# Performance work log

Measured on AMD Instinct MI355X. Metric: run time of the kernel, lower is better.

## Reference

```python
import jax, jax.numpy as jnp
import numpy as np

B, N, C, O, K, D = 32, 2048, 64, 64, 3, 16

def setup_inputs() -> dict:
    key = jax.random.key(0)
    ks = jax.random.split(key, 6)
    x = jax.random.normal(ks[0], (B, N, C), dtype=jnp.float32)
    node_embeddings = jax.random.normal(ks[1], (N, D), dtype=jnp.float32)
    adj_m = jax.random.uniform(ks[2], (N, N), dtype=jnp.float32)
    weights_pool = jax.random.normal(ks[3], (D, K, C, O), dtype=jnp.float32) * 0.1
    bias_pool = jax.random.normal(ks[4], (D, O), dtype=jnp.float32) * 0.1
    sa_weight = jax.random.normal(ks[5], (N, 2 * N), dtype=jnp.float32) * (1.0 / np.sqrt(2 * N))
    return {"x": x, "node_embeddings": node_embeddings, "adj_m": adj_m,
            "weights_pool": weights_pool, "bias_pool": bias_pool, "sa_weight": sa_weight}

def reference(x, node_embeddings, adj_m, weights_pool, bias_pool, sa_weight):
    n = node_embeddings.shape[0]
    # learned adaptive adjacency [N,N]
    supports = jax.nn.softmax(jax.nn.relu(node_embeddings @ node_embeddings.T), axis=1)
    # SpatialAttention: 1x1 conv over 2N channels == matmul with [N,2N] weight
    z = jnp.concatenate([supports, adj_m], axis=1) @ sa_weight.T  # [N,N]
    s2 = jax.nn.sigmoid(z)
    supports = s2 * adj_m + (1.0 - s2) * supports
    # Chebyshev polynomial basis
    support_set = [jnp.eye(n, dtype=supports.dtype), supports]
    for _ in range(2, K):
        support_set.append(2.0 * supports @ support_set[-1] - support_set[-2])
    supports_k = jnp.stack(support_set, axis=0)  # [K,N,N]
    # per-node generated weights/bias from embeddings
    weights = jnp.einsum('nd,dkio->nkio', node_embeddings, weights_pool)  # [N,K,C,O]
    bias = node_embeddings @ bias_pool  # [N,O]
    # graph conv: aggregate then per-node matmul
    x_g = jnp.einsum('knm,bmc->bnkc', supports_k, x)  # [B,N,K,C]
    x_gconv = jnp.einsum('bnki,nkio->bno', x_g, weights) + bias  # [B,N,O]
    return x_gconv
```

## Files before the change

kernel.cpp:

```cpp
#include <hip/hip_runtime.h>


typedef unsigned short u16;
typedef float f32x4 __attribute__((ext_vector_type(4)));
typedef __bf16 bf16x8 __attribute__((ext_vector_type(8)));
typedef unsigned short u16x8 __attribute__((ext_vector_type(8)));

#define PSTRIDE ((size_t)2048 * 2048)

__device__ __forceinline__ u16 f2bf(float f) {
    unsigned u = __float_as_uint(f);
    u += 0x7FFFu + ((u >> 16) & 1u);
    return (u16)(u >> 16);
}
__device__ __forceinline__ float bf2f(u16 h) {
    return __uint_as_float((unsigned)h << 16);
}
__device__ __forceinline__ void gl_lds16(const void* g, void* l) {
    __builtin_amdgcn_global_load_lds(
        (const __attribute__((address_space(1))) unsigned*)g,
        (__attribute__((address_space(3))) unsigned*)l, 16, 0, 0);
}

__global__ __launch_bounds__(256)
void preamble(const float* __restrict__ E, const float* __restrict__ adj,
              const float* __restrict__ saw, const float* __restrict__ x,
              const float* __restrict__ Wp, const float* __restrict__ bp,
              float* __restrict__ zf, u16* __restrict__ Acat,
              u16* __restrict__ sawb, u16* __restrict__ xtT,
              u16* __restrict__ Wpb, float* __restrict__ bias) {
    __shared__ u16 t[64][65];
    __shared__ float Bp[1024];
    const int bid = blockIdx.x, tid = threadIdx.x;

    if (bid < 256) {
        const int c0 = (bid & 31) * 64, r0 = (bid >> 5) * 256;
        const int r = r0 + tid;
        const float4* Er = (const float4*)(E + (size_t)r * 16);
        float4 e0 = Er[0], e1 = Er[1], e2 = Er[2], e3 = Er[3];
        *(float4*)(Bp + tid * 4) = *(const float4*)(E + (size_t)c0 * 16 + tid * 4);
        __syncthreads();
        float* zr = zf + (size_t)r * 2048 + c0;
#pragma unroll
        for (int cc = 0; cc < 4; ++cc) {
            float acc[16];
#pragma unroll
            for (int c = 0; c < 16; ++c) {
                const float* bp = Bp + (cc * 16 + c) * 16;
                float s = 0.f;
                s = fmaf(e0.x, bp[0], s);  s = fmaf(e0.y, bp[1], s);
                s = fmaf(e0.z, bp[2], s);  s = fmaf(e0.w, bp[3], s);
                s = fmaf(e1.x, bp[4], s);  s = fmaf(e1.y, bp[5], s);
                s = fmaf(e1.z, bp[6], s);  s = fmaf(e1.w, bp[7], s);
                s = fmaf(e2.x, bp[8], s);  s = fmaf(e2.y, bp[9], s);
                s = fmaf(e2.z, bp[10], s); s = fmaf(e2.w, bp[11], s);
                s = fmaf(e3.x, bp[12], s); s = fmaf(e3.y, bp[13], s);
                s = fmaf(e3.z, bp[14], s); s = fmaf(e3.w, bp[15], s);
                acc[c] = fmaxf(s, 0.f);
            }
#pragma unroll
            for (int q = 0; q < 4; ++q)
                *(float4*)(zr + cc * 16 + q * 4) =
                    make_float4(acc[q * 4], acc[q * 4 + 1], acc[q * 4 + 2], acc[q * 4 + 3]);
        }
    } else if (bid < 4352) {
        size_t j = ((size_t)(bid - 256) * 256 + tid) * 4;
        float4 v = *(const float4*)(adj + j);
        int n = (int)(j >> 11), c = (int)(j & 2047);
        ushort4 o = make_ushort4(f2bf(v.x), f2bf(v.y), f2bf(v.z), f2bf(v.w));
        *(ushort4*)(Acat + (size_t)n * 4096 + 2048 + c) = o;
    } else if (bid < 12544) {
        size_t j = ((size_t)(bid - 4352) * 256 + tid) * 4;
        float4 v = *(const float4*)(saw + j);
        ushort4 o = make_ushort4(f2bf(v.x), f2bf(v.y), f2bf(v.z), f2bf(v.w));
        *(ushort4*)(sawb + j) = o;
    } else if (bid < 13568) {
        int local = bid - 12544;
        int m0 = (local & 31) * 64, b = local >> 5;
        int c = tid & 63, g = tid >> 6;
#pragma unroll
        for (int r = 0; r < 16; ++r) {
            int mm = g * 16 + r;
            t[mm][c] = f2bf(x[((size_t)b * 2048 + m0 + mm) * 64 + c]);
        }
        __syncthreads();
#pragma unroll
        for (int r = 0; r < 16; ++r) {
            int cc = g * 16 + r;
            xtT[((size_t)b * 64 + cc) * 2048 + m0 + c] = t[c][cc];
        }
    } else {
        int local = bid - 13568;
        if (local < 16) {
            const int d = local;
            const float* base = Wp + (size_t)d * 12288;
            for (int idx = tid; idx < 12288; idx += 256) {
                int o = idx / 192, ki = idx - o * 192;
                int k = ki >> 6, i = ki & 63;
                float v;
                if (k == 0)      v = base[i * 64 + o] - base[2 * 4096 + i * 64 + o];
                else if (k == 1) v = base[4096 + i * 64 + o];
                else             v = 2.f * base[2 * 4096 + i * 64 + o];
                Wpb[(size_t)(d * 64 + o) * 192 + ki] = f2bf(v);
            }
        } else {
            const int nb = local - 16;
#pragma unroll
            for (int it = 0; it < 8; ++it) {
                int idx = tid + it * 256;
                int n = nb * 32 + (idx >> 6), o = idx & 63;
                float s = 0.f;
#pragma unroll
                for (int d = 0; d < 16; ++d) s = fmaf(E[n * 16 + d], bp[d * 64 + o], s);
                bias[(size_t)n * 64 + o] = s;
            }
        }
    }
}

__global__ __launch_bounds__(256)
void softmax_rows(const float* __restrict__ zf, u16* __restrict__ Acat) {
    __shared__ float red[4];
    const int n = blockIdx.x, tid = threadIdx.x;
    const int lane = tid & 63, wave = tid >> 6;
    const float* zr = zf + (size_t)n * 2048;
    float4 a = *(const float4*)(zr + tid * 8);
    float4 b = *(const float4*)(zr + tid * 8 + 4);
    float mx = fmaxf(fmaxf(fmaxf(a.x, a.y), fmaxf(a.z, a.w)),
                     fmaxf(fmaxf(b.x, b.y), fmaxf(b.z, b.w)));
    for (int off = 32; off; off >>= 1) mx = fmaxf(mx, __shfl_down(mx, off, 64));
    if (lane == 0) red[wave] = mx;
    __syncthreads();
    mx = fmaxf(fmaxf(red[0], red[1]), fmaxf(red[2], red[3]));
    __syncthreads();
    float v[8] = {__expf(a.x - mx), __expf(a.y - mx), __expf(a.z - mx), __expf(a.w - mx),
                  __expf(b.x - mx), __expf(b.y - mx), __expf(b.z - mx), __expf(b.w - mx)};
    float sum = v[0] + v[1] + v[2] + v[3] + v[4] + v[5] + v[6] + v[7];
    for (int off = 32; off; off >>= 1) sum += __shfl_down(sum, off, 64);
    if (lane == 0) red[wave] = sum;
    __syncthreads();
    sum = red[0] + red[1] + red[2] + red[3];
    float inv = 1.f / sum;
    u16* orow = Acat + (size_t)n * 4096 + tid * 8;
    *(ushort4*)orow = make_ushort4(f2bf(v[0] * inv), f2bf(v[1] * inv),
                                   f2bf(v[2] * inv), f2bf(v[3] * inv));
    *(ushort4*)(orow + 4) = make_ushort4(f2bf(v[4] * inv), f2bf(v[5] * inv),
                                         f2bf(v[6] * inv), f2bf(v[7] * inv));
}

__global__ __launch_bounds__(256, 3)
void gemm_bt(const u16* __restrict__ A, const u16* __restrict__ Bt,
             u16* __restrict__ Cp, int M, int N, int K, int Kh) {
    __shared__ alignas(16) u16 As[128 * 64];
    __shared__ alignas(16) u16 Bs[128 * 64];
    const int tid = threadIdx.x, lane = tid & 63, wave = tid >> 6;
    const int m0 = blockIdx.y * 128, n0 = blockIdx.x * 128;
    const int wm = (wave >> 1) * 64, wn = (wave & 1) * 64;
    const int kbeg = blockIdx.z * Kh, kend = kbeg + Kh;
    const int ml = lane & 15, c0l = lane >> 4;
    f32x4 acc[4][4] = {};

    int baseA[4], mskA[4], baseB[4], mskB[4];
#pragma unroll
    for (int i = 0; i < 4; ++i) { int m = wm + i * 16 + ml; baseA[i] = m * 8; mskA[i] = m & 7; }
#pragma unroll
    for (int j = 0; j < 4; ++j) { int nn = wn + j * 16 + ml; baseB[j] = nn * 8; mskB[j] = nn & 7; }

    for (int k0 = kbeg; k0 < kend; k0 += 64) {
#pragma unroll
        for (int r = 0; r < 4; ++r) {
            int s = wave * 64 + r * 256 + lane;
            int row = s >> 3, gc = (s & 7) ^ (row & 7);
            gl_lds16(A + (size_t)(m0 + row) * K + k0 + gc * 8, As + (size_t)s * 8);
        }
#pragma unroll
        for (int r = 0; r < 4; ++r) {
            int s = wave * 64 + r * 256 + lane;
            int row = s >> 3, gc = (s & 7) ^ (row & 7);
            gl_lds16(Bt + (size_t)(n0 + row) * K + k0 + gc * 8, Bs + (size_t)s * 8);
        }
        __syncthreads();
#pragma unroll
        for (int ks4 = 0; ks4 < 8; ks4 += 4) {
            bf16x8 af[4], bv[4];
#pragma unroll
            for (int i = 0; i < 4; ++i)
                af[i] = *(const bf16x8*)(As + (baseA[i] + ((c0l + ks4) ^ mskA[i])) * 8);
#pragma unroll
            for (int j = 0; j < 4; ++j)
                bv[j] = *(const bf16x8*)(Bs + (baseB[j] + ((c0l + ks4) ^ mskB[j])) * 8);
#pragma unroll
            for (int i = 0; i < 4; ++i)
#pragma unroll
                for (int j = 0; j < 4; ++j)
                    acc[i][j] = __builtin_amdgcn_mfma_f32_16x16x32_bf16(af[i], bv[j], acc[i][j], 0, 0, 0);
        }
        __syncthreads();
    }

    const int col_l = lane & 15, row_l = (lane >> 4) * 4;
    u16* Cz = Cp + (size_t)blockIdx.z * M * N;
#pragma unroll
    for (int i = 0; i < 4; ++i)
#pragma unroll
        for (int j = 0; j < 4; ++j)
#pragma unroll
            for (int r = 0; r < 4; ++r) {
                int row = m0 + wm + i * 16 + row_l + r;
                int col = n0 + wn + j * 16 + col_l;
                Cz[(size_t)row * N + col] = f2bf(acc[i][j][r]);
            }
}

__global__ __launch_bounds__(256)
void reduce_z(const u16* __restrict__ p, const u16* __restrict__ Acat,
              u16* __restrict__ S) {
    size_t j = ((size_t)blockIdx.x * 256 + threadIdx.x) * 4;
    ushort4 p0 = *(const ushort4*)(p + j);
    ushort4 p1 = *(const ushort4*)(p + PSTRIDE + j);
    ushort4 p2 = *(const ushort4*)(p + 2 * PSTRIDE + j);
    ushort4 p3 = *(const ushort4*)(p + 3 * PSTRIDE + j);
    int row = (int)(j >> 11), col = (int)(j & 2047);
    ushort4 sp = *(const ushort4*)(Acat + (size_t)row * 4096 + col);
    ushort4 ad = *(const ushort4*)(Acat + (size_t)row * 4096 + 2048 + col);
    float z0 = bf2f(p0.x) + bf2f(p1.x) + bf2f(p2.x) + bf2f(p3.x);
    float z1 = bf2f(p0.y) + bf2f(p1.y) + bf2f(p2.y) + bf2f(p3.y);
    float z2 = bf2f(p0.z) + bf2f(p1.z) + bf2f(p2.z) + bf2f(p3.z);
    float z3 = bf2f(p0.w) + bf2f(p1.w) + bf2f(p2.w) + bf2f(p3.w);
    float s0 = 1.f / (1.f + __expf(-z0)), s1 = 1.f / (1.f + __expf(-z1));
    float s2 = 1.f / (1.f + __expf(-z2)), s3 = 1.f / (1.f + __expf(-z3));
    ushort4 o = make_ushort4(
        f2bf(s0 * bf2f(ad.x) + (1.f - s0) * bf2f(sp.x)),
        f2bf(s1 * bf2f(ad.y) + (1.f - s1) * bf2f(sp.y)),
        f2bf(s2 * bf2f(ad.z) + (1.f - s2) * bf2f(sp.z)),
        f2bf(s3 * bf2f(ad.w) + (1.f - s3) * bf2f(sp.w)));
    *(ushort4*)(S + j) = o;
}

__global__ __launch_bounds__(256)
void reduceT(const u16* __restrict__ p, u16* __restrict__ xg1b,
             u16* __restrict__ xg1T) {
    __shared__ u16 t[64][68];
    int bx = blockIdx.x * 64, by = blockIdx.y * 64;
    int cg = threadIdx.x & 15, rg = threadIdx.x >> 4;
    int b = bx >> 6;
#pragma unroll
    for (int rr = 0; rr < 4; ++rr) {
        int row = rg * 4 + rr;
        size_t idx = (size_t)(by + row) * 2048 + bx + cg * 4;
        ushort4 q0 = *(const ushort4*)(p + idx);
        ushort4 q1 = *(const ushort4*)(p + PSTRIDE + idx);
        ushort4 q2 = *(const ushort4*)(p + 2 * PSTRIDE + idx);
        ushort4 q3 = *(const ushort4*)(p + 3 * PSTRIDE + idx);
        ushort4 v = make_ushort4(
            f2bf(bf2f(q0.x) + bf2f(q1.x) + bf2f(q2.x) + bf2f(q3.x)),
            f2bf(bf2f(q0.y) + bf2f(q1.y) + bf2f(q2.y) + bf2f(q3.y)),
            f2bf(bf2f(q0.z) + bf2f(q1.z) + bf2f(q2.z) + bf2f(q3.z)),
            f2bf(bf2f(q0.w) + bf2f(q1.w) + bf2f(q2.w) + bf2f(q3.w)));
        *(ushort4*)(xg1b + ((size_t)b * 2048 + by + row) * 64 + cg * 4) = v;
        *(ushort4*)(&t[row][cg * 4]) = v;
    }
    __syncthreads();
    int c = threadIdx.x & 63, g = threadIdx.x >> 6;
#pragma unroll
    for (int r = 0; r < 16; ++r) {
        int row = g * 16 + r;
        xg1T[(size_t)(bx + row) * 2048 + by + c] = t[c][row];
    }
}

__global__ __launch_bounds__(256, 2)
void gconv_mfma(const float* __restrict__ x, const u16* __restrict__ xg1,
                const u16* __restrict__ p, const u16* __restrict__ Wpb,
                const float* __restrict__ bias, const float* __restrict__ E,
                float* __restrict__ out) {
    __shared__ alignas(16) u16 As[128 * 192];
    __shared__ float El[16 * 128];
    const int tid = threadIdx.x, lane = tid & 63, wave = tid >> 6;
    const int m0 = blockIdx.x * 128, nb = m0 & 2047, bB = m0 >> 11;
    const int wm = (wave >> 1) * 64, wn = (wave & 1) * 32;
    const int ml = lane & 15, c0l = lane >> 4;
    const int col_l = lane & 15, rl = (lane >> 4) * 4;

#pragma unroll
    for (int it = 0; it < 12; ++it) {
        int s = tid + it * 256;
        int row = s / 24, sc = s - row * 24;
        int gc = (sc & 24) | ((sc ^ row) & 7);
        int grow = m0 + row;
        u16x8 v;
        if (gc < 8) {
            const float* xp = x + (size_t)grow * 64 + gc * 8;
            float4 a = *(const float4*)xp, b4 = *(const float4*)(xp + 4);
            v[0] = f2bf(a.x);  v[1] = f2bf(a.y);  v[2] = f2bf(a.z);  v[3] = f2bf(a.w);
            v[4] = f2bf(b4.x); v[5] = f2bf(b4.y); v[6] = f2bf(b4.z); v[7] = f2bf(b4.w);
        } else if (gc < 16) {
            v = *(const u16x8*)(xg1 + (size_t)grow * 64 + (gc & 7) * 8);
        } else {
            int n = grow & 2047, c8 = (gc & 7) * 8;
            const u16* pp = p + (size_t)n * 2048 + bB * 64 + c8;
            u16x8 q0 = *(const u16x8*)pp;
            u16x8 q1 = *(const u16x8*)(pp + PSTRIDE);
            u16x8 q2 = *(const u16x8*)(pp + 2 * PSTRIDE);
            u16x8 q3 = *(const u16x8*)(pp + 3 * PSTRIDE);
#pragma unroll
            for (int tt = 0; tt < 8; ++tt)
                v[tt] = f2bf(bf2f(q0[tt]) + bf2f(q1[tt]) + bf2f(q2[tt]) + bf2f(q3[tt]));
        }
        *(u16x8*)(As + (size_t)s * 8) = v;
    }
#pragma unroll
    for (int it = 0; it < 8; ++it) {
        int idx = tid + it * 256;
        El[idx] = E[(size_t)(nb + (idx & 127)) * 16 + (idx >> 7)];
    }
    f32x4 oacc[4][2];
#pragma unroll
    for (int i = 0; i < 4; ++i)
#pragma unroll
        for (int j = 0; j < 2; ++j)
#pragma unroll
            for (int r = 0; r < 4; ++r)
                oacc[i][j][r] = bias[(size_t)(nb + wm + i * 16 + rl + r) * 64 + wn + j * 16 + col_l];
    __syncthreads();

    bf16x8 af[4][6];
#pragma unroll
    for (int i = 0; i < 4; ++i) {
        int m = wm + i * 16 + ml, base = m * 24, msk = m & 7;
#pragma unroll
        for (int ks = 0; ks < 6; ++ks) {
            int c = c0l + ks * 4;
            af[i][ks] = *(const bf16x8*)(As + (base + ((c & 24) | ((c ^ msk) & 7))) * 8);
        }
    }
    __syncthreads();

#pragma unroll
    for (int it = 0; it < 6; ++it) {
        int s = tid + it * 256;
        int row = s / 24, sc = s - row * 24;
        int gc = (sc & 24) | ((sc ^ row) & 7);
        gl_lds16(Wpb + (size_t)row * 192 + gc * 8, As + (size_t)s * 8);
    }

    for (int d = 0; d < 16; ++d) {
        __syncthreads();
        if (d < 15) {
            u16* nbuf = As + ((d + 1) & 1) * (64 * 192);
#pragma unroll
            for (int it = 0; it < 6; ++it) {
                int s = tid + it * 256;
                int row = s / 24, sc = s - row * 24;
                int gc = (sc & 24) | ((sc ^ row) & 7);
                gl_lds16(Wpb + (size_t)((d + 1) * 64 + row) * 192 + gc * 8, nbuf + (size_t)s * 8);
            }
        }
        const u16* Bs = As + (d & 1) * (64 * 192);
        f32x4 tmp[4][2] = {};
#pragma unroll
        for (int ks = 0; ks < 6; ++ks) {
            bf16x8 bv[2];
#pragma unroll
            for (int j = 0; j < 2; ++j) {
                int o = wn + j * 16 + ml, msk = o & 7, c = c0l + ks * 4;
                bv[j] = *(const bf16x8*)(Bs + (o * 24 + ((c & 24) | ((c ^ msk) & 7))) * 8);
            }
#pragma unroll
            for (int i = 0; i < 4; ++i)
#pragma unroll
                for (int j = 0; j < 2; ++j)
                    tmp[i][j] = __builtin_amdgcn_mfma_f32_16x16x32_bf16(af[i][ks], bv[j], tmp[i][j], 0, 0, 0);
        }
#pragma unroll
        for (int i = 0; i < 4; ++i)
#pragma unroll
            for (int r = 0; r < 4; ++r) {
                float ev = El[d * 128 + wm + i * 16 + rl + r];
#pragma unroll
                for (int j = 0; j < 2; ++j)
                    oacc[i][j][r] = fmaf(ev, tmp[i][j][r], oacc[i][j][r]);
            }
    }
#pragma unroll
    for (int i = 0; i < 4; ++i)
#pragma unroll
        for (int j = 0; j < 2; ++j)
#pragma unroll
            for (int r = 0; r < 4; ++r)
                out[(size_t)(m0 + wm + i * 16 + rl + r) * 64 + wn + j * 16 + col_l] = oacc[i][j][r];
}

extern "C" void kernel_launch(void* const* d_in, const int* in_sizes, int n_in,
                              void* d_out, int out_size, void* d_ws, size_t ws_size,
                              hipStream_t stream) {
    const float* x   = (const float*)d_in[0];
    const float* E   = (const float*)d_in[1];
    const float* adj = (const float*)d_in[2];
    const float* Wp  = (const float*)d_in[3];
    const float* bp  = (const float*)d_in[4];
    const float* saw = (const float*)d_in[5];
    float* out = (float*)d_out;

    char* ws = (char*)d_ws;
    const size_t MB = 1u << 20;
    u16*   Acat  = (u16*)(ws);
    u16*   sawb  = (u16*)(ws + 16 * MB);
    u16*   XtT   = (u16*)(ws + 32 * MB);
    u16*   Wpb   = (u16*)(ws + 40 * MB);
    float* bias  = (float*)(ws + 41 * MB);
    float* zf    = (float*)(ws + 48 * MB);
    u16*   part  = (u16*)(ws + 48 * MB);
    u16*   S_bf  = (u16*)(ws + 16 * MB);
    u16*   xg1T  = (u16*)(ws + 24 * MB);
    u16*   xg1b  = (u16*)(ws);

    preamble<<<13648, 256, 0, stream>>>(E, adj, saw, x, Wp, bp, zf, Acat, sawb, XtT, Wpb, bias);
    softmax_rows<<<2048, 256, 0, stream>>>(zf, Acat);

    gemm_bt<<<dim3(16, 16, 4), 256, 0, stream>>>(Acat, sawb, part, 2048, 2048, 4096, 1024);
    reduce_z<<<4096, 256, 0, stream>>>(part, Acat, S_bf);
    gemm_bt<<<dim3(16, 16, 4), 256, 0, stream>>>(S_bf, XtT, part, 2048, 2048, 2048, 512);
    reduceT<<<dim3(32, 32), 256, 0, stream>>>(part, xg1b, xg1T);
    gemm_bt<<<dim3(16, 16, 4), 256, 0, stream>>>(S_bf, xg1T, part, 2048, 2048, 2048, 512);

    gconv_mfma<<<512, 256, 0, stream>>>(x, xg1b, part, Wpb, bias, E, out);
}
```

Before: 281.7 us.

## Load gconv A and W fragments directly from global memory into registers, dropping LDS staging

The gconv_mfma kernel no longer stages the concatenated A tile (x, xg1, summed p) and the per-d weight tiles in shared memory. Each lane now loads its MFMA fragments straight from global memory into registers, and the double-buffered global_load_lds pipeline and its barriers are removed. The El lookup becomes a vector load, and the d loop is unrolled by two. This cuts LDS footprint and synchronization, which may allow higher occupancy, at the cost of redundant and less coalesced global/L2 reads of Wpb across waves and blocks.

```diff
diff --git a/kernel.cpp b/kernel.cpp
--- a/kernel.cpp
+++ b/kernel.cpp
@@ -46,16 +46,16 @@
             float acc[16];
 #pragma unroll
             for (int c = 0; c < 16; ++c) {
-                const float* bp = Bp + (cc * 16 + c) * 16;
+                const float* bp2 = Bp + (cc * 16 + c) * 16;
                 float s = 0.f;
-                s = fmaf(e0.x, bp[0], s);  s = fmaf(e0.y, bp[1], s);
-                s = fmaf(e0.z, bp[2], s);  s = fmaf(e0.w, bp[3], s);
-                s = fmaf(e1.x, bp[4], s);  s = fmaf(e1.y, bp[5], s);
-                s = fmaf(e1.z, bp[6], s);  s = fmaf(e1.w, bp[7], s);
-                s = fmaf(e2.x, bp[8], s);  s = fmaf(e2.y, bp[9], s);
-                s = fmaf(e2.z, bp[10], s); s = fmaf(e2.w, bp[11], s);
-                s = fmaf(e3.x, bp[12], s); s = fmaf(e3.y, bp[13], s);
-                s = fmaf(e3.z, bp[14], s); s = fmaf(e3.w, bp[15], s);
+                s = fmaf(e0.x, bp2[0], s);  s = fmaf(e0.y, bp2[1], s);
+                s = fmaf(e0.z, bp2[2], s);  s = fmaf(e0.w, bp2[3], s);
+                s = fmaf(e1.x, bp2[4], s);  s = fmaf(e1.y, bp2[5], s);
+                s = fmaf(e1.z, bp2[6], s);  s = fmaf(e1.w, bp2[7], s);
+                s = fmaf(e2.x, bp2[8], s);  s = fmaf(e2.y, bp2[9], s);
+                s = fmaf(e2.z, bp2[10], s); s = fmaf(e2.w, bp2[11], s);
+                s = fmaf(e3.x, bp2[12], s); s = fmaf(e3.y, bp2[13], s);
+                s = fmaf(e3.z, bp2[14], s); s = fmaf(e3.w, bp2[15], s);
                 acc[c] = fmaxf(s, 0.f);
             }
 #pragma unroll
@@ -274,8 +274,7 @@
                 const u16* __restrict__ p, const u16* __restrict__ Wpb,
                 const float* __restrict__ bias, const float* __restrict__ E,
                 float* __restrict__ out) {
-    __shared__ alignas(16) u16 As[128 * 192];
-    __shared__ float El[16 * 128];
+    __shared__ alignas(16) float El[16 * 128];
     const int tid = threadIdx.x, lane = tid & 63, wave = tid >> 6;
     const int m0 = blockIdx.x * 128, nb = m0 & 2047, bB = m0 >> 11;
     const int wm = (wave >> 1) * 64, wn = (wave & 1) * 32;
@@ -283,37 +282,44 @@
     const int col_l = lane & 15, rl = (lane >> 4) * 4;
 
 #pragma unroll
-    for (int it = 0; it < 12; ++it) {
-        int s = tid + it * 256;
-        int row = s / 24, sc = s - row * 24;
-        int gc = (sc & 24) | ((sc ^ row) & 7);
-        int grow = m0 + row;
-        u16x8 v;
-        if (gc < 8) {
-            const float* xp = x + (size_t)grow * 64 + gc * 8;
+    for (int it = 0; it < 8; ++it) {
+        int idx = tid + it * 256;
+        El[idx] = E[(size_t)(nb + (idx & 127)) * 16 + (idx >> 7)];
+    }
+    __syncthreads();
+
+    bf16x8 af[4][6];
+#pragma unroll
+    for (int i = 0; i < 4; ++i) {
+        const int row = m0 + wm + i * 16 + ml;
+        const int n = row & 2047;
+#pragma unroll
+        for (int ks = 0; ks < 2; ++ks) {
+            const float* xp = x + (size_t)row * 64 + (c0l + ks * 4) * 8;
             float4 a = *(const float4*)xp, b4 = *(const float4*)(xp + 4);
+            u16x8 v;
             v[0] = f2bf(a.x);  v[1] = f2bf(a.y);  v[2] = f2bf(a.z);  v[3] = f2bf(a.w);
             v[4] = f2bf(b4.x); v[5] = f2bf(b4.y); v[6] = f2bf(b4.z); v[7] = f2bf(b4.w);
-        } else if (gc < 16) {
-            v = *(const u16x8*)(xg1 + (size_t)grow * 64 + (gc & 7) * 8);
-        } else {
-            int n = grow & 2047, c8 = (gc & 7) * 8;
-            const u16* pp = p + (size_t)n * 2048 + bB * 64 + c8;
+            af[i][ks] = __builtin_bit_cast(bf16x8, v);
+        }
+#pragma unroll
+        for (int ks = 2; ks < 4; ++ks)
+            af[i][ks] = *(const bf16x8*)(xg1 + (size_t)row * 64 + (c0l + ks * 4 - 8) * 8);
+#pragma unroll
+        for (int ks = 4; ks < 6; ++ks) {
+            const u16* pp = p + (size_t)n * 2048 + bB * 64 + (c0l + ks * 4 - 16) * 8;
             u16x8 q0 = *(const u16x8*)pp;
             u16x8 q1 = *(const u16x8*)(pp + PSTRIDE);
             u16x8 q2 = *(const u16x8*)(pp + 2 * PSTRIDE);
             u16x8 q3 = *(const u16x8*)(pp + 3 * PSTRIDE);
+            u16x8 v;
 #pragma unroll
             for (int tt = 0; tt < 8; ++tt)
                 v[tt] = f2bf(bf2f(q0[tt]) + bf2f(q1[tt]) + bf2f(q2[tt]) + bf2f(q3[tt]));
-        }
-        *(u16x8*)(As + (size_t)s * 8) = v;
-    }
-#pragma unroll
-    for (int it = 0; it < 8; ++it) {
-        int idx = tid + it * 256;
-        El[idx] = E[(size_t)(nb + (idx & 127)) * 16 + (idx >> 7)];
-    }
+            af[i][ks] = __builtin_bit_cast(bf16x8, v);
+        }
+    }
+
     f32x4 oacc[4][2];
 #pragma unroll
     for (int i = 0; i < 4; ++i)
@@ -322,65 +328,34 @@
 #pragma unroll
             for (int r = 0; r < 4; ++r)
                 oacc[i][j][r] = bias[(size_t)(nb + wm + i * 16 + rl + r) * 64 + wn + j * 16 + col_l];
-    __syncthreads();
-
-    bf16x8 af[4][6];
-#pragma unroll
-    for (int i = 0; i < 4; ++i) {
-        int m = wm + i * 16 + ml, base = m * 24, msk = m & 7;
-#pragma unroll
-        for (int ks = 0; ks < 6; ++ks) {
-            int c = c0l + ks * 4;
-            af[i][ks] = *(const bf16x8*)(As + (base + ((c & 24) | ((c ^ msk) & 7))) * 8);
-        }
-    }
-    __syncthreads();
-
-#pragma unroll
-    for (int it = 0; it < 6; ++it) {
-        int s = tid + it * 256;
-        int row = s / 24, sc = s - row * 24;
-        int gc = (sc & 24) | ((sc ^ row) & 7);
-        gl_lds16(Wpb + (size_t)row * 192 + gc * 8, As + (size_t)s * 8);
-    }
-
+
+#pragma unroll 2
     for (int d = 0; d < 16; ++d) {
-        __syncthreads();
-        if (d < 15) {
-            u16* nbuf = As + ((d + 1) & 1) * (64 * 192);
-#pragma unroll
-            for (int it = 0; it < 6; ++it) {
-                int s = tid + it * 256;
-                int row = s / 24, sc = s - row * 24;
-                int gc = (sc & 24) | ((sc ^ row) & 7);
-                gl_lds16(Wpb + (size_t)((d + 1) * 64 + row) * 192 + gc * 8, nbuf + (size_t)s * 8);
-            }
-        }
-        const u16* Bs = As + (d & 1) * (64 * 192);
+        bf16x8 bv[2][6];
+#pragma unroll
+        for (int j = 0; j < 2; ++j) {
+            const u16* wp = Wpb + (size_t)(d * 64 + wn + j * 16 + ml) * 192 + c0l * 8;
+#pragma unroll
+            for (int ks = 0; ks < 6; ++ks)
+                bv[j][ks] = *(const bf16x8*)(wp + ks * 32);
+        }
         f32x4 tmp[4][2] = {};
 #pragma unroll
-        for (int ks = 0; ks < 6; ++ks) {
-            bf16x8 bv[2];
-#pragma unroll
-            for (int j = 0; j < 2; ++j) {
-                int o = wn + j * 16 + ml, msk = o & 7, c = c0l + ks * 4;
-                bv[j] = *(const bf16x8*)(Bs + (o * 24 + ((c & 24) | ((c ^ msk) & 7))) * 8);
-            }
+        for (int ks = 0; ks < 6; ++ks)
 #pragma unroll
             for (int i = 0; i < 4; ++i)
 #pragma unroll
                 for (int j = 0; j < 2; ++j)
-                    tmp[i][j] = __builtin_amdgcn_mfma_f32_16x16x32_bf16(af[i][ks], bv[j], tmp[i][j], 0, 0, 0);
-        }
-#pragma unroll
-        for (int i = 0; i < 4; ++i)
-#pragma unroll
-            for (int r = 0; r < 4; ++r) {
-                float ev = El[d * 128 + wm + i * 16 + rl + r];
+                    tmp[i][j] = __builtin_amdgcn_mfma_f32_16x16x32_bf16(af[i][ks], bv[j][ks], tmp[i][j], 0, 0, 0);
+#pragma unroll
+        for (int i = 0; i < 4; ++i) {
+            f32x4 ev = *(const f32x4*)(El + d * 128 + wm + i * 16 + rl);
+#pragma unroll
+            for (int r = 0; r < 4; ++r)
 #pragma unroll
                 for (int j = 0; j < 2; ++j)
-                    oacc[i][j][r] = fmaf(ev, tmp[i][j][r], oacc[i][j][r]);
-            }
+                    oacc[i][j][r] = fmaf(ev[r], tmp[i][j][r], oacc[i][j][r]);
+        }
     }
 #pragma unroll
     for (int i = 0; i < 4; ++i)
```

After: 304.1 us. 7.9% more time.
